# Kernel tuning notes

Measured on AMD Instinct MI355X. Metric: run time of the kernel, lower is better.

The kernel has to match this reference:

```python
import jax, jax.numpy as jnp
import numpy as np

INPUT_SIZE = 64
HIDDEN = 512
NUM_CLASSES = 10


def setup_inputs() -> dict:
    key = jax.random.key(0)
    ks = jax.random.split(key, 9)
    B, T = 1024, 256
    bound_lstm = 1.0 / np.sqrt(HIDDEN)
    bound_lin = 1.0 / np.sqrt(HIDDEN)
    x = jax.random.normal(ks[0], (B, T * INPUT_SIZE), dtype=jnp.float32)
    h0 = jax.random.normal(ks[1], (B, HIDDEN), dtype=jnp.float32)
    c0 = jax.random.normal(ks[2], (B, HIDDEN), dtype=jnp.float32)
    W_ih = jax.random.uniform(ks[3], (4 * HIDDEN, INPUT_SIZE), jnp.float32, -bound_lstm, bound_lstm)
    W_hh = jax.random.uniform(ks[4], (4 * HIDDEN, HIDDEN), jnp.float32, -bound_lstm, bound_lstm)
    b_ih = jax.random.uniform(ks[5], (4 * HIDDEN,), jnp.float32, -bound_lstm, bound_lstm)
    b_hh = jax.random.uniform(ks[6], (4 * HIDDEN,), jnp.float32, -bound_lstm, bound_lstm)
    W_lin = jax.random.uniform(ks[7], (NUM_CLASSES, HIDDEN), jnp.float32, -bound_lin, bound_lin)
    b_lin = jax.random.uniform(ks[8], (NUM_CLASSES,), jnp.float32, -bound_lin, bound_lin)
    return {"x": x, "h0": h0, "c0": c0, "W_ih": W_ih, "W_hh": W_hh,
            "b_ih": b_ih, "b_hh": b_hh, "W_lin": W_lin, "b_lin": b_lin}


def _lstm_forward(x, h0, c0, W_ih, W_hh, b_ih, b_hh, W_lin, b_lin):
    B = x.shape[0]
    T = x.shape[1] // INPUT_SIZE
    # [B, T*in] -> [T, B, in]; torch.split along dim 1 gives contiguous chunks
    xs = x.reshape(B, T, INPUT_SIZE).transpose(1, 0, 2)
    # precompute input projections for all steps: [T, B, 4H]
    gates_x = jnp.einsum('tbi,gi->tbg', xs, W_ih) + b_ih + b_hh

    def step(carry, gx):
        h, c = carry
        gates = gx + h @ W_hh.T  # [B, 4H], torch gate order i,f,g,o
        i, f, g, o = jnp.split(gates, 4, axis=-1)
        i = jax.nn.sigmoid(i)
        f = jax.nn.sigmoid(f)
        g = jnp.tanh(g)
        o = jax.nn.sigmoid(o)
        c_new = f * c + i * g
        h_new = o * jnp.tanh(c_new)
        return (h_new, c_new), None

    (hT, cT), _ = jax.lax.scan(step, (h0, c0), gates_x)
    preds = hT @ W_lin.T + b_lin  # [B, 10]
    return preds


def reference(x, h0, c0, W_ih, W_hh, b_ih, b_hh, W_lin, b_lin):
    return _lstm_forward(x, h0, c0, W_ih, W_hh, b_ih, b_hh, W_lin, b_lin)
```

## Files before the change

kernel.cpp:

```cpp
#include <hip/hip_runtime.h>
#include <hip/hip_bf16.h>


#define TST   256
#define BATCH 1024
#define HID   512
#define INSZ  64
#define NCLS  10
#define LDSTR 584

typedef _Float16 f16x8  __attribute__((ext_vector_type(8)));
typedef float    f32x16 __attribute__((ext_vector_type(16)));
typedef unsigned long long u64;

__device__ __forceinline__ float fast_rcp(float x) {
    return __builtin_amdgcn_rcpf(x);
}

__device__ __forceinline__ float tanh_f(float x) {
    return 2.0f * fast_rcp(1.0f + __expf(-2.0f * x)) - 1.0f;
}

__device__ __forceinline__ f16x8 cvt8(float4 a, float4 b) {
    f16x8 o;
    o[0] = (_Float16)a.x; o[1] = (_Float16)a.y; o[2] = (_Float16)a.z; o[3] = (_Float16)a.w;
    o[4] = (_Float16)b.x; o[5] = (_Float16)b.y; o[6] = (_Float16)b.z; o[7] = (_Float16)b.w;
    return o;
}

__device__ __forceinline__ u64 cvt4_u64(float4 a) {
    _Float16 h[4] = {(_Float16)a.x, (_Float16)a.y, (_Float16)a.z, (_Float16)a.w};
    u64 r;
    __builtin_memcpy(&r, h, 8);
    return r;
}

template <int CTRL>
__device__ __forceinline__ float dpp_f(float v) {
    return __builtin_bit_cast(float,
        __builtin_amdgcn_mov_dpp(__builtin_bit_cast(int, v), CTRL, 0xF, 0xF, true));
}
template <int CTRL>
__device__ __forceinline__ unsigned dpp_u(unsigned v) {
    return (unsigned)__builtin_amdgcn_mov_dpp((int)v, CTRL, 0xF, 0xF, true);
}

__global__ __launch_bounds__(256, 1) void lstm_persist(
    const float* __restrict__ x,   const float* __restrict__ h0,
    const float* __restrict__ c0,  const float* __restrict__ Wih,
    const float* __restrict__ Whh, const float* __restrict__ bih,
    const float* __restrict__ bhh, _Float16* __restrict__ hb,
    unsigned* __restrict__ bar)
{
    __shared__ __align__(16) _Float16 As[32][LDSTR];

    const int tid   = threadIdx.x;
    const int lane  = tid & 63;
    const int w     = tid >> 6;
    const int l31   = lane & 31;
    const int khalf = (lane >> 5) * 8;
    const int g  = (int)(blockIdx.x >> 3);
    const int jb = (int)(blockIdx.x & 7);
    const int m0 = g * 32;
    const int j0 = jb * 64;
    unsigned* flg = bar + g * 64;

    const int gate = l31 & 3;
    int jcol[2], nrow[2];
    #pragma unroll
    for (int nt = 0; nt < 2; ++nt) {
        int np = w * 64 + nt * 32 + l31;
        jcol[nt] = j0 + (np >> 2);
        nrow[nt] = gate * HID + jcol[nt];
    }

    f16x8 bfr[2][36];
    #pragma unroll
    for (int nt = 0; nt < 2; ++nt)
        #pragma unroll
        for (int kt = 0; kt < 36; ++kt) {
            const int k0 = kt * 16 + khalf;
            const float* p = (kt < 32) ? (Whh + (size_t)nrow[nt] * HID + k0)
                                       : (Wih + (size_t)nrow[nt] * INSZ + (k0 - HID));
            float4 f0 = ((const float4*)p)[0];
            float4 f1 = ((const float4*)p)[1];
            bfr[nt][kt] = cvt8(f0, f1);
        }
    float bsv[2];
    bsv[0] = bih[nrow[0]] + bhh[nrow[0]];
    bsv[1] = bih[nrow[1]] + bhh[nrow[1]];
    const float s   = (gate == 2) ? 2.0f : 1.0f;
    const int rowhi = (lane >> 5) * 4;

    float cr[2][16];
    #pragma unroll
    for (int nt = 0; nt < 2; ++nt)
        #pragma unroll
        for (int r = 0; r < 16; ++r) {
            int row = (r & 3) + 8 * (r >> 2) + rowhi;
            cr[nt][r] = c0[(size_t)(m0 + row) * HID + jcol[nt]];
        }

    const int rr = tid >> 3;
    const int q  = tid & 7;

    for (int t = 0; t < TST; ++t) {
        const _Float16* rb = hb + (size_t)((t + 2) % 3) * (BATCH * HID);
        _Float16*       wb = hb + (size_t)(t % 3) * (BATCH * HID);

        float4 x0, x1;
        {
            const float* xp = x + (size_t)(m0 + rr) * (TST * INSZ) + t * INSZ + q * 8;
            x0 = ((const float4*)xp)[0];
            x1 = ((const float4*)xp)[1];
        }
        if (t == 0) {
            u64 hv[16];
            #pragma unroll
            for (int u = 0; u < 16; ++u) {
                float4 f = *(const float4*)(h0 + (size_t)(m0 + rr) * HID + q * 4 + u * 32);
                hv[u] = cvt4_u64(f);
            }
            #pragma unroll
            for (int u = 0; u < 16; ++u)
                *(u64*)&As[rr][q * 4 + u * 32] = hv[u];
        } else {
            const unsigned tgt = (unsigned)t;
            int spins = 0;
            while (true) {
                unsigned v = __hip_atomic_load(flg + (lane & 31),
                                               __ATOMIC_RELAXED, __HIP_MEMORY_SCOPE_AGENT);
                if (__all((int)(v >= tgt))) break;
                if (++spins > (1 << 14)) break;
                __builtin_amdgcn_s_sleep(1);
            }
            __atomic_signal_fence(__ATOMIC_SEQ_CST);
            const u64* rbq = (const u64*)(rb + (size_t)(m0 + rr) * HID);
            u64 hv[16];
            #pragma unroll
            for (int u = 0; u < 16; ++u)
                hv[u] = __hip_atomic_load(&rbq[q + u * 8],
                                          __ATOMIC_RELAXED, __HIP_MEMORY_SCOPE_AGENT);
            #pragma unroll
            for (int u = 0; u < 16; ++u)
                *(u64*)&As[rr][q * 4 + u * 32] = hv[u];
        }
        *(f16x8*)&As[rr][512 + q * 8] = cvt8(x0, x1);
        __syncthreads();

        f32x16 acc[2];
        #pragma unroll
        for (int i = 0; i < 16; ++i) { acc[0][i] = 0.0f; acc[1][i] = 0.0f; }
        #pragma unroll
        for (int kt = 0; kt < 36; ++kt) {
            f16x8 af = *(const f16x8*)&As[l31][kt * 16 + khalf];
            acc[0] = __builtin_amdgcn_mfma_f32_32x32x16_f16(af, bfr[0][kt], acc[0], 0, 0, 0);
            acc[1] = __builtin_amdgcn_mfma_f32_32x32x16_f16(af, bfr[1][kt], acc[1], 0, 0, 0);
        }

        #pragma unroll
        for (int nt = 0; nt < 2; ++nt) {
            #pragma unroll
            for (int r = 0; r < 16; ++r) {
                float v = acc[nt][r] + bsv[nt];
                float e = __expf(-s * v);
                float act = s * fast_rcp(1.0f + e) - (s - 1.0f);
                float fu = dpp_f<0xB1>(act);
                float gu = dpp_f<0x4E>(act);
                float ou = dpp_f<0x1B>(act);
                float cn = fu * cr[nt][r] + act * gu;
                cr[nt][r] = cn;
                float hn = ou * tanh_f(cn);
                unsigned hu = (unsigned)__builtin_bit_cast(unsigned short, (_Float16)hn);
                unsigned pk = hu | (dpp_u<0x104>(hu) << 16);
                u64 v4 = (u64)pk | ((u64)dpp_u<0x108>(pk) << 32);
                if ((l31 & 15) == 0) {
                    int row = (r & 3) + 8 * (r >> 2) + rowhi;
                    (void)__hip_atomic_exchange(
                        (u64*)&wb[(size_t)(m0 + row) * HID + jcol[nt]],
                        v4, __ATOMIC_RELAXED, __HIP_MEMORY_SCOPE_AGENT);
                }
            }
        }

        asm volatile("s_waitcnt vmcnt(0)" ::: "memory");
        if (lane == 0)
            (void)__hip_atomic_exchange(flg + (jb * 4 + w), (unsigned)(t + 1),
                                        __ATOMIC_RELAXED, __HIP_MEMORY_SCOPE_AGENT);
    }
}

__global__ __launch_bounds__(256) void final_kernel(
    const _Float16* __restrict__ h, const float* __restrict__ Wl,
    const float* __restrict__ bl, float* __restrict__ out)
{
    int i = blockIdx.x * 256 + threadIdx.x;
    if (i >= BATCH * NCLS) return;
    int b = i / NCLS, c = i - b * NCLS;
    const f16x8* hp = (const f16x8*)(h + (size_t)b * HID);
    const float4* wp = (const float4*)(Wl + (size_t)c * HID);
    float sacc = bl[c];
    #pragma unroll 4
    for (int k8 = 0; k8 < HID / 8; ++k8) {
        f16x8 hv = hp[k8];
        float4 w0 = wp[2 * k8], w1 = wp[2 * k8 + 1];
        sacc += (float)hv[0] * w0.x + (float)hv[1] * w0.y +
                (float)hv[2] * w0.z + (float)hv[3] * w0.w +
                (float)hv[4] * w1.x + (float)hv[5] * w1.y +
                (float)hv[6] * w1.z + (float)hv[7] * w1.w;
    }
    out[i] = sacc;
}

extern "C" void kernel_launch(void* const* d_in, const int* in_sizes, int n_in,
                              void* d_out, int out_size, void* d_ws, size_t ws_size,
                              hipStream_t stream)
{
    const float* x    = (const float*)d_in[0];
    const float* h0   = (const float*)d_in[1];
    const float* c0   = (const float*)d_in[2];
    const float* Wih  = (const float*)d_in[3];
    const float* Whh  = (const float*)d_in[4];
    const float* bih  = (const float*)d_in[5];
    const float* bhh  = (const float*)d_in[6];
    const float* Wlin = (const float*)d_in[7];
    const float* blin = (const float*)d_in[8];
    float* out = (float*)d_out;

    unsigned* bar = (unsigned*)d_ws;
    _Float16* hb  = (_Float16*)((char*)d_ws + 8192);

    hipMemsetAsync(d_ws, 0, 8192, stream);

    lstm_persist<<<256, 256, 0, stream>>>(x, h0, c0, Wih, Whh, bih, bhh, hb, bar);

    final_kernel<<<(BATCH * NCLS + 255) / 256, 256, 0, stream>>>(hb, Wlin, blin, out);
}
```

Measured before the change: 1.743 ms.

## Interleave two half-batch tiles per block to overlap recurrence barrier waits

Each persistent block now owns two independent 16-row batch tiles taken from the two halves of the batch. Each tile has its own LDS buffer and its own flag set, and the block processes the tiles one after the other within each timestep. The aim is that while one tile's neighbours finish publishing h, the block works on the other tile, which hides inter-block synchronization latency. In exchange, every tile still runs the full 32-row MFMA sequence with only 16 valid rows, so the matrix work per step doubles. It also adds an extra __syncthreads per tile, and the h and flag writes use plain atomic stores instead of exchanges.

```diff
diff --git a/kernel.cpp b/kernel.cpp
--- a/kernel.cpp
+++ b/kernel.cpp
@@ -52,18 +52,18 @@
     const float* __restrict__ bhh, _Float16* __restrict__ hb,
     unsigned* __restrict__ bar)
 {
-    __shared__ __align__(16) _Float16 As[32][LDSTR];
+    __shared__ __align__(16) _Float16 As[2][32][LDSTR];
 
     const int tid   = threadIdx.x;
     const int lane  = tid & 63;
     const int w     = tid >> 6;
     const int l31   = lane & 31;
     const int khalf = (lane >> 5) * 8;
-    const int g  = (int)(blockIdx.x >> 3);
+    const int p  = (int)(blockIdx.x >> 3);
     const int jb = (int)(blockIdx.x & 7);
-    const int m0 = g * 32;
     const int j0 = jb * 64;
-    unsigned* flg = bar + g * 64;
+    const int m0T[2]      = { p * 16, 512 + p * 16 };
+    unsigned* const flgT[2] = { bar + p * 32, bar + (32 + p) * 32 };
 
     const int gate = l31 & 3;
     int jcol[2], nrow[2];
@@ -80,10 +80,10 @@
         #pragma unroll
         for (int kt = 0; kt < 36; ++kt) {
             const int k0 = kt * 16 + khalf;
-            const float* p = (kt < 32) ? (Whh + (size_t)nrow[nt] * HID + k0)
-                                       : (Wih + (size_t)nrow[nt] * INSZ + (k0 - HID));
-            float4 f0 = ((const float4*)p)[0];
-            float4 f1 = ((const float4*)p)[1];
+            const float* ptr = (kt < 32) ? (Whh + (size_t)nrow[nt] * HID + k0)
+                                         : (Wih + (size_t)nrow[nt] * INSZ + (k0 - HID));
+            float4 f0 = ((const float4*)ptr)[0];
+            float4 f1 = ((const float4*)ptr)[1];
             bfr[nt][kt] = cvt8(f0, f1);
         }
     float bsv[2];
@@ -92,101 +92,110 @@
     const float s   = (gate == 2) ? 2.0f : 1.0f;
     const int rowhi = (lane >> 5) * 4;
 
-    float cr[2][16];
+    float cr[2][2][8];
     #pragma unroll
-    for (int nt = 0; nt < 2; ++nt)
+    for (int task = 0; task < 2; ++task)
         #pragma unroll
-        for (int r = 0; r < 16; ++r) {
-            int row = (r & 3) + 8 * (r >> 2) + rowhi;
-            cr[nt][r] = c0[(size_t)(m0 + row) * HID + jcol[nt]];
-        }
-
-    const int rr = tid >> 3;
-    const int q  = tid & 7;
+        for (int nt = 0; nt < 2; ++nt)
+            #pragma unroll
+            for (int r = 0; r < 8; ++r) {
+                int row = (r & 3) + 8 * (r >> 2) + rowhi;
+                cr[task][nt][r] = c0[(size_t)(m0T[task] + row) * HID + jcol[nt]];
+            }
+
+    const int rr = tid >> 4;
+    const int q  = tid & 15;
 
     for (int t = 0; t < TST; ++t) {
         const _Float16* rb = hb + (size_t)((t + 2) % 3) * (BATCH * HID);
         _Float16*       wb = hb + (size_t)(t % 3) * (BATCH * HID);
 
-        float4 x0, x1;
-        {
-            const float* xp = x + (size_t)(m0 + rr) * (TST * INSZ) + t * INSZ + q * 8;
-            x0 = ((const float4*)xp)[0];
-            x1 = ((const float4*)xp)[1];
+        #pragma unroll
+        for (int task = 0; task < 2; ++task) {
+            unsigned* flg = flgT[task];
+            const int mb  = m0T[task];
+
+            float4 x0 = *(const float4*)(x + (size_t)(mb + rr) * (TST * INSZ)
+                                           + t * INSZ + q * 4);
+
+            if (t == 0) {
+                u64 hv[8];
+                #pragma unroll
+                for (int u = 0; u < 8; ++u) {
+                    float4 f = *(const float4*)(h0 + (size_t)(mb + rr) * HID
+                                                  + q * 4 + u * 64);
+                    hv[u] = cvt4_u64(f);
+                }
+                #pragma unroll
+                for (int u = 0; u < 8; ++u)
+                    *(u64*)&As[task][rr][q * 4 + u * 64] = hv[u];
+            } else {
+                const unsigned tgt = (unsigned)t;
+                int spins = 0;
+                while (true) {
+                    unsigned v = __hip_atomic_load(flg + (lane & 31),
+                                                   __ATOMIC_RELAXED,
+                                                   __HIP_MEMORY_SCOPE_AGENT);
+                    if (__all((int)(v >= tgt))) break;
+                    if (++spins > (1 << 14)) break;
+                    __builtin_amdgcn_s_sleep(1);
+                }
+                __atomic_signal_fence(__ATOMIC_SEQ_CST);
+                const u64* rbq = (const u64*)(rb + (size_t)(mb + rr) * HID);
+                u64 hv[8];
+                #pragma unroll
+                for (int u = 0; u < 8; ++u)
+                    hv[u] = __hip_atomic_load(&rbq[q + u * 16],
+                                              __ATOMIC_RELAXED,
+                                              __HIP_MEMORY_SCOPE_AGENT);
+                #pragma unroll
+                for (int u = 0; u < 8; ++u)
+                    *(u64*)&As[task][rr][q * 4 + u * 64] = hv[u];
+            }
+            *(u64*)&As[task][rr][512 + q * 4] = cvt4_u64(x0);
+            __syncthreads();
+
+            f32x16 acc[2];
+            #pragma unroll
+            for (int i = 0; i < 16; ++i) { acc[0][i] = 0.0f; acc[1][i] = 0.0f; }
+            #pragma unroll
+            for (int kt = 0; kt < 36; ++kt) {
+                f16x8 af = *(const f16x8*)&As[task][l31][kt * 16 + khalf];
+                acc[0] = __builtin_amdgcn_mfma_f32_32x32x16_f16(af, bfr[0][kt], acc[0], 0, 0, 0);
+                acc[1] = __builtin_amdgcn_mfma_f32_32x32x16_f16(af, bfr[1][kt], acc[1], 0, 0, 0);
+            }
+
+            #pragma unroll
+            for (int nt = 0; nt < 2; ++nt) {
+                #pragma unroll
+                for (int r = 0; r < 8; ++r) {
+                    float v = acc[nt][r] + bsv[nt];
+                    float e = __expf(-s * v);
+                    float act = s * fast_rcp(1.0f + e) - (s - 1.0f);
+                    float fu = dpp_f<0xB1>(act);
+                    float gu = dpp_f<0x4E>(act);
+                    float ou = dpp_f<0x1B>(act);
+                    float cn = fu * cr[task][nt][r] + act * gu;
+                    cr[task][nt][r] = cn;
+                    float hn = ou * tanh_f(cn);
+                    unsigned hu = (unsigned)__builtin_bit_cast(unsigned short, (_Float16)hn);
+                    unsigned pk = hu | (dpp_u<0x104>(hu) << 16);
+                    u64 v4 = (u64)pk | ((u64)dpp_u<0x108>(pk) << 32);
+                    if ((l31 & 15) == 0) {
+                        int row = (r & 3) + 8 * (r >> 2) + rowhi;
+                        __hip_atomic_store(
+                            (u64*)&wb[(size_t)(mb + row) * HID + jcol[nt]],
+                            v4, __ATOMIC_RELAXED, __HIP_MEMORY_SCOPE_AGENT);
+                    }
+                }
+            }
+
+            asm volatile("s_waitcnt vmcnt(0)" ::: "memory");
+            if (lane == 0)
+                __hip_atomic_store(flg + (jb * 4 + w), (unsigned)(t + 1),
+                                   __ATOMIC_RELAXED, __HIP_MEMORY_SCOPE_AGENT);
+            __syncthreads();
         }
-        if (t == 0) {
-            u64 hv[16];
-            #pragma unroll
-            for (int u = 0; u < 16; ++u) {
-                float4 f = *(const float4*)(h0 + (size_t)(m0 + rr) * HID + q * 4 + u * 32);
-                hv[u] = cvt4_u64(f);
-            }
-            #pragma unroll
-            for (int u = 0; u < 16; ++u)
-                *(u64*)&As[rr][q * 4 + u * 32] = hv[u];
-        } else {
-            const unsigned tgt = (unsigned)t;
-            int spins = 0;
-            while (true) {
-                unsigned v = __hip_atomic_load(flg + (lane & 31),
-                                               __ATOMIC_RELAXED, __HIP_MEMORY_SCOPE_AGENT);
-                if (__all((int)(v >= tgt))) break;
-                if (++spins > (1 << 14)) break;
-                __builtin_amdgcn_s_sleep(1);
-            }
-            __atomic_signal_fence(__ATOMIC_SEQ_CST);
-            const u64* rbq = (const u64*)(rb + (size_t)(m0 + rr) * HID);
-            u64 hv[16];
-            #pragma unroll
-            for (int u = 0; u < 16; ++u)
-                hv[u] = __hip_atomic_load(&rbq[q + u * 8],
-                                          __ATOMIC_RELAXED, __HIP_MEMORY_SCOPE_AGENT);
-            #pragma unroll
-            for (int u = 0; u < 16; ++u)
-                *(u64*)&As[rr][q * 4 + u * 32] = hv[u];
-        }
-        *(f16x8*)&As[rr][512 + q * 8] = cvt8(x0, x1);
-        __syncthreads();
-
-        f32x16 acc[2];
-        #pragma unroll
-        for (int i = 0; i < 16; ++i) { acc[0][i] = 0.0f; acc[1][i] = 0.0f; }
-        #pragma unroll
-        for (int kt = 0; kt < 36; ++kt) {
-            f16x8 af = *(const f16x8*)&As[l31][kt * 16 + khalf];
-            acc[0] = __builtin_amdgcn_mfma_f32_32x32x16_f16(af, bfr[0][kt], acc[0], 0, 0, 0);
-            acc[1] = __builtin_amdgcn_mfma_f32_32x32x16_f16(af, bfr[1][kt], acc[1], 0, 0, 0);
-        }
-
-        #pragma unroll
-        for (int nt = 0; nt < 2; ++nt) {
-            #pragma unroll
-            for (int r = 0; r < 16; ++r) {
-                float v = acc[nt][r] + bsv[nt];
-                float e = __expf(-s * v);
-                float act = s * fast_rcp(1.0f + e) - (s - 1.0f);
-                float fu = dpp_f<0xB1>(act);
-                float gu = dpp_f<0x4E>(act);
-                float ou = dpp_f<0x1B>(act);
-                float cn = fu * cr[nt][r] + act * gu;
-                cr[nt][r] = cn;
-                float hn = ou * tanh_f(cn);
-                unsigned hu = (unsigned)__builtin_bit_cast(unsigned short, (_Float16)hn);
-                unsigned pk = hu | (dpp_u<0x104>(hu) << 16);
-                u64 v4 = (u64)pk | ((u64)dpp_u<0x108>(pk) << 32);
-                if ((l31 & 15) == 0) {
-                    int row = (r & 3) + 8 * (r >> 2) + rowhi;
-                    (void)__hip_atomic_exchange(
-                        (u64*)&wb[(size_t)(m0 + row) * HID + jcol[nt]],
-                        v4, __ATOMIC_RELAXED, __HIP_MEMORY_SCOPE_AGENT);
-                }
-            }
-        }
-
-        asm volatile("s_waitcnt vmcnt(0)" ::: "memory");
-        if (lane == 0)
-            (void)__hip_atomic_exchange(flg + (jb * 4 + w), (unsigned)(t + 1),
-                                        __ATOMIC_RELAXED, __HIP_MEMORY_SCOPE_AGENT);
     }
 }
 
```

Result: slower. 2.353 ms (+35.0%).

## Replace flag barrier with per-word step tags embedded in hidden-state buffer

Applied to the files above, without the earlier changes.

Drops the separate per-group flag array and the wait-then-publish barrier. Each 64-bit store now carries two fp16 hidden values in its low half and the step index in its high half, so readers spin on the data itself until every tag matches. This removes the vmcnt drain and the flag round trip on every step. In exchange it doubles the bytes per hidden-state read, requires memsetting the whole triple buffer, and moves polling onto the full data loads.

```diff
diff --git a/kernel.cpp b/kernel.cpp
--- a/kernel.cpp
+++ b/kernel.cpp
@@ -28,13 +28,6 @@
     return o;
 }
 
-__device__ __forceinline__ u64 cvt4_u64(float4 a) {
-    _Float16 h[4] = {(_Float16)a.x, (_Float16)a.y, (_Float16)a.z, (_Float16)a.w};
-    u64 r;
-    __builtin_memcpy(&r, h, 8);
-    return r;
-}
-
 template <int CTRL>
 __device__ __forceinline__ float dpp_f(float v) {
     return __builtin_bit_cast(float,
@@ -49,8 +42,7 @@
     const float* __restrict__ x,   const float* __restrict__ h0,
     const float* __restrict__ c0,  const float* __restrict__ Wih,
     const float* __restrict__ Whh, const float* __restrict__ bih,
-    const float* __restrict__ bhh, _Float16* __restrict__ hb,
-    unsigned* __restrict__ bar)
+    const float* __restrict__ bhh, u64* __restrict__ hb)
 {
     __shared__ __align__(16) _Float16 As[32][LDSTR];
 
@@ -63,7 +55,6 @@
     const int jb = (int)(blockIdx.x & 7);
     const int m0 = g * 32;
     const int j0 = jb * 64;
-    unsigned* flg = bar + g * 64;
 
     const int gate = l31 & 3;
     int jcol[2], nrow[2];
@@ -105,8 +96,8 @@
     const int q  = tid & 7;
 
     for (int t = 0; t < TST; ++t) {
-        const _Float16* rb = hb + (size_t)((t + 2) % 3) * (BATCH * HID);
-        _Float16*       wb = hb + (size_t)(t % 3) * (BATCH * HID);
+        const u64* rb = hb + (size_t)((t + 2) % 3) * (BATCH * HID / 2);
+        u64*       wb = hb + (size_t)(t % 3) * (BATCH * HID / 2);
 
         float4 x0, x1;
         {
@@ -115,35 +106,35 @@
             x1 = ((const float4*)xp)[1];
         }
         if (t == 0) {
-            u64 hv[16];
             #pragma unroll
             for (int u = 0; u < 16; ++u) {
                 float4 f = *(const float4*)(h0 + (size_t)(m0 + rr) * HID + q * 4 + u * 32);
-                hv[u] = cvt4_u64(f);
+                _Float16 h4[4] = {(_Float16)f.x, (_Float16)f.y, (_Float16)f.z, (_Float16)f.w};
+                u64 r8; __builtin_memcpy(&r8, h4, 8);
+                *(u64*)&As[rr][q * 4 + u * 32] = r8;
             }
-            #pragma unroll
-            for (int u = 0; u < 16; ++u)
-                *(u64*)&As[rr][q * 4 + u * 32] = hv[u];
         } else {
             const unsigned tgt = (unsigned)t;
+            const u64* rbq = rb + (size_t)(m0 + rr) * 256;
+            u64 hv[32];
             int spins = 0;
             while (true) {
-                unsigned v = __hip_atomic_load(flg + (lane & 31),
-                                               __ATOMIC_RELAXED, __HIP_MEMORY_SCOPE_AGENT);
-                if (__all((int)(v >= tgt))) break;
+                unsigned bad = 0;
+                #pragma unroll
+                for (int u = 0; u < 32; ++u)
+                    hv[u] = __hip_atomic_load(&rbq[q + u * 8],
+                                              __ATOMIC_RELAXED, __HIP_MEMORY_SCOPE_AGENT);
+                #pragma unroll
+                for (int u = 0; u < 32; ++u)
+                    bad |= ((unsigned)(hv[u] >> 32)) ^ tgt;
+                if (__all((int)(bad == 0))) break;
                 if (++spins > (1 << 14)) break;
-                __builtin_amdgcn_s_sleep(1);
+                __builtin_amdgcn_s_sleep(8);
             }
             __atomic_signal_fence(__ATOMIC_SEQ_CST);
-            const u64* rbq = (const u64*)(rb + (size_t)(m0 + rr) * HID);
-            u64 hv[16];
             #pragma unroll
-            for (int u = 0; u < 16; ++u)
-                hv[u] = __hip_atomic_load(&rbq[q + u * 8],
-                                          __ATOMIC_RELAXED, __HIP_MEMORY_SCOPE_AGENT);
-            #pragma unroll
-            for (int u = 0; u < 16; ++u)
-                *(u64*)&As[rr][q * 4 + u * 32] = hv[u];
+            for (int u = 0; u < 32; ++u)
+                *(unsigned*)&As[rr][(q + u * 8) * 2] = (unsigned)hv[u];
         }
         *(f16x8*)&As[rr][512 + q * 8] = cvt8(x0, x1);
         __syncthreads();
@@ -158,6 +149,7 @@
             acc[1] = __builtin_amdgcn_mfma_f32_32x32x16_f16(af, bfr[1][kt], acc[1], 0, 0, 0);
         }
 
+        const u64 tag64 = ((u64)(unsigned)(t + 1)) << 32;
         #pragma unroll
         for (int nt = 0; nt < 2; ++nt) {
             #pragma unroll
@@ -173,41 +165,35 @@
                 float hn = ou * tanh_f(cn);
                 unsigned hu = (unsigned)__builtin_bit_cast(unsigned short, (_Float16)hn);
                 unsigned pk = hu | (dpp_u<0x104>(hu) << 16);
-                u64 v4 = (u64)pk | ((u64)dpp_u<0x108>(pk) << 32);
-                if ((l31 & 15) == 0) {
+                if ((l31 & 7) == 0) {
                     int row = (r & 3) + 8 * (r >> 2) + rowhi;
-                    (void)__hip_atomic_exchange(
-                        (u64*)&wb[(size_t)(m0 + row) * HID + jcol[nt]],
-                        v4, __ATOMIC_RELAXED, __HIP_MEMORY_SCOPE_AGENT);
+                    __hip_atomic_store(
+                        wb + ((size_t)(m0 + row) * HID + jcol[nt]) / 2,
+                        (u64)pk | tag64,
+                        __ATOMIC_RELAXED, __HIP_MEMORY_SCOPE_AGENT);
                 }
             }
         }
-
-        asm volatile("s_waitcnt vmcnt(0)" ::: "memory");
-        if (lane == 0)
-            (void)__hip_atomic_exchange(flg + (jb * 4 + w), (unsigned)(t + 1),
-                                        __ATOMIC_RELAXED, __HIP_MEMORY_SCOPE_AGENT);
     }
 }
 
 __global__ __launch_bounds__(256) void final_kernel(
-    const _Float16* __restrict__ h, const float* __restrict__ Wl,
+    const u64* __restrict__ h, const float* __restrict__ Wl,
     const float* __restrict__ bl, float* __restrict__ out)
 {
     int i = blockIdx.x * 256 + threadIdx.x;
     if (i >= BATCH * NCLS) return;
     int b = i / NCLS, c = i - b * NCLS;
-    const f16x8* hp = (const f16x8*)(h + (size_t)b * HID);
-    const float4* wp = (const float4*)(Wl + (size_t)c * HID);
+    const u64* hp = h + (size_t)b * (HID / 2);
+    const float2* wp = (const float2*)(Wl + (size_t)c * HID);
     float sacc = bl[c];
-    #pragma unroll 4
-    for (int k8 = 0; k8 < HID / 8; ++k8) {
-        f16x8 hv = hp[k8];
-        float4 w0 = wp[2 * k8], w1 = wp[2 * k8 + 1];
-        sacc += (float)hv[0] * w0.x + (float)hv[1] * w0.y +
-                (float)hv[2] * w0.z + (float)hv[3] * w0.w +
-                (float)hv[4] * w1.x + (float)hv[5] * w1.y +
-                (float)hv[6] * w1.z + (float)hv[7] * w1.w;
+    #pragma unroll 8
+    for (int k2 = 0; k2 < HID / 2; ++k2) {
+        unsigned lo = (unsigned)hp[k2];
+        _Float16 h0v = __builtin_bit_cast(_Float16, (unsigned short)(lo & 0xFFFF));
+        _Float16 h1v = __builtin_bit_cast(_Float16, (unsigned short)(lo >> 16));
+        float2 wv = wp[k2];
+        sacc += (float)h0v * wv.x + (float)h1v * wv.y;
     }
     out[i] = sacc;
 }
@@ -227,12 +213,11 @@
     const float* blin = (const float*)d_in[8];
     float* out = (float*)d_out;
 
-    unsigned* bar = (unsigned*)d_ws;
-    _Float16* hb  = (_Float16*)((char*)d_ws + 8192);
-
-    hipMemsetAsync(d_ws, 0, 8192, stream);
-
-    lstm_persist<<<256, 256, 0, stream>>>(x, h0, c0, Wih, Whh, bih, bhh, hb, bar);
+    u64* hb = (u64*)d_ws;
+
+    hipMemsetAsync(d_ws, 0, 3 * (size_t)(BATCH * HID / 2) * 8, stream);
+
+    lstm_persist<<<256, 256, 0, stream>>>(x, h0, c0, Wih, Whh, bih, bhh, hb);
 
     final_kernel<<<(BATCH * NCLS + 255) / 256, 256, 0, stream>>>(hb, Wlin, blin, out);
 }
```

Result: no change. 1.750 ms (+0.4%).
